# Optimization experiments

Measured on AMD Instinct MI355X. Metric: run time of the kernel, lower is better.

## Reference

```python
import jax, jax.numpy as jnp
import numpy as np

N_EMBD = 1024
NUM_EXPERTS = 8
TOP_K = 2
HIDDEN = 2048  # n_embd * hidden_mult(2)
AUX_COEF = 0.01
B, S = 4, 2048


def setup_inputs() -> dict:
    key = jax.random.key(0)
    k_x, k_g, k_w1, k_w2 = jax.random.split(key, 4)
    x = jax.random.normal(k_x, (B, S, N_EMBD), dtype=jnp.float32)
    # router gate: Linear(n_embd, num_experts, bias=False) -> weight (E, D), applied as x @ W^T
    gate_w = jax.random.uniform(k_g, (NUM_EXPERTS, N_EMBD), dtype=jnp.float32,
                                minval=-1.0 / np.sqrt(N_EMBD), maxval=1.0 / np.sqrt(N_EMBD))
    w1 = jax.random.uniform(k_w1, (NUM_EXPERTS, N_EMBD, HIDDEN), dtype=jnp.float32,
                            minval=-1.0 / np.sqrt(N_EMBD), maxval=1.0 / np.sqrt(N_EMBD))
    w2 = jax.random.uniform(k_w2, (NUM_EXPERTS, HIDDEN, N_EMBD), dtype=jnp.float32,
                            minval=-1.0 / np.sqrt(HIDDEN), maxval=1.0 / np.sqrt(HIDDEN))
    return {"x": x, "gate_w": gate_w, "w1": w1, "w2": w2}


def reference(x, gate_w, w1, w2):
    batch, seq, d = x.shape
    # router (token-level, no noise / eval path)
    router_logits = jnp.einsum('bsd,ed->bse', x, gate_w)          # (B,S,E)
    router_probs = jax.nn.softmax(router_logits, axis=-1)
    top_k_probs, top_k_indices = jax.lax.top_k(router_probs, TOP_K)  # (B,S,K)
    top_k_probs = top_k_probs / jnp.sum(top_k_probs, axis=-1, keepdims=True)

    # dense all-expert FFN (matches torch einsum pattern)
    x_flat = x.reshape(-1, d)                                      # (N,D), N=B*S
    hidden = jnp.einsum('nd,edh->neh', x_flat, w1)                 # (N,E,H)
    hidden = jax.nn.relu(hidden)
    expert_out = jnp.einsum('neh,ehd->ned', hidden, w2)            # (N,E,D)
    expert_out = expert_out.reshape(batch, seq, NUM_EXPERTS, d)    # (B,S,E,D)

    # gather selected experts and combine
    idx = top_k_indices[..., None]                                 # (B,S,K,1)
    selected = jnp.take_along_axis(expert_out, idx, axis=2)        # (B,S,K,D)
    output = jnp.sum(selected * top_k_probs[..., None], axis=2)    # (B,S,D)

    # load-balancing aux loss (Switch style)
    probs_flat = router_probs.reshape(-1, NUM_EXPERTS)             # (N,E)
    top_expert = jnp.argmax(probs_flat, axis=-1)                   # (N,)
    f = jnp.mean(jax.nn.one_hot(top_expert, NUM_EXPERTS, dtype=probs_flat.dtype), axis=0)
    P = jnp.mean(probs_flat, axis=0)
    aux_loss = AUX_COEF * NUM_EXPERTS * jnp.sum(f * P)
    return output, aux_loss
```

## Files before the change

kernel.cpp:

```cpp
#include <hip/hip_runtime.h>
#include <hip/hip_bf16.h>
#include <stdint.h>

#define N_TOK 8192
#define DIM   1024
#define HID   2048
#define NEXP  8
#define RB    256

typedef __bf16 bf16x8 __attribute__((ext_vector_type(8)));
typedef float  f32x4  __attribute__((ext_vector_type(4)));
typedef unsigned short u16x8 __attribute__((ext_vector_type(8)));
typedef unsigned short u16x4 __attribute__((ext_vector_type(4)));

__device__ __forceinline__ float bits2f(unsigned short u) {
    union { unsigned int i; float f; } c; c.i = ((unsigned int)u) << 16; return c.f;
}
__device__ __forceinline__ unsigned short f2bfbits(float f) {
    __hip_bfloat16 h = __float2bfloat16(f);
    return *(unsigned short*)&h;
}

__device__ __forceinline__ void load_lds16(const void* g, void* l) {
    __builtin_amdgcn_global_load_lds(
        (const __attribute__((address_space(1))) void*)g,
        (__attribute__((address_space(3))) void*)l,
        16, 0, 0);
}

#define VMW(Nv) asm volatile("s_waitcnt vmcnt(" #Nv ")" ::: "memory")
#define BARv()  asm volatile("s_barrier" ::: "memory")
#define LGKM0() do { asm volatile("s_waitcnt lgkmcnt(0)" ::: "memory"); \
                     __builtin_amdgcn_sched_barrier(0); } while (0)

__global__ __launch_bounds__(256) void fused_pre_k(
    const float* __restrict__ x,
    const float* __restrict__ gate,
    const float* __restrict__ w1,
    const float* __restrict__ w2,
    int* __restrict__ epack, float* __restrict__ pw,
    unsigned short* __restrict__ xb,
    int* __restrict__ H0, int* __restrict__ H1, float* __restrict__ Pblk,
    unsigned short* __restrict__ w1t, unsigned short* __restrict__ w2t)
{
    __shared__ __align__(16) union {
        struct { float gw[NEXP][16][64]; int h0[NEXP]; int h1[NEXP]; float p[NEXP]; } r;
        unsigned short tile[64][72];
    } S;
    const int tid = threadIdx.x;
    const int bx  = blockIdx.x;

    if (bx < RB) {
        if (tid < NEXP) { S.r.h0[tid] = 0; S.r.h1[tid] = 0; S.r.p[tid] = 0.f; }
        for (int idx = tid; idx < NEXP * DIM; idx += 256) {
            int e = idx >> 10, rem = idx & 1023, i = rem >> 6, l = rem & 63;
            S.r.gw[e][i][l] = gate[e * DIM + l * 16 + i];
        }
        __syncthreads();
        int w = tid >> 6, lane = tid & 63;
        float prAcc[NEXP];
        #pragma unroll
        for (int e = 0; e < NEXP; ++e) prAcc[e] = 0.f;
        for (int it = 0; it < 8; ++it) {
            int token = bx * 32 + w * 8 + it;
            const float* xr = x + (size_t)token * DIM + lane * 16;
            float xv[16];
            #pragma unroll
            for (int q = 0; q < 4; ++q) {
                float4 v = *(const float4*)(xr + q * 4);
                xv[q * 4 + 0] = v.x; xv[q * 4 + 1] = v.y; xv[q * 4 + 2] = v.z; xv[q * 4 + 3] = v.w;
            }
            {
                u16x8 o0, o1;
                #pragma unroll
                for (int i = 0; i < 8; ++i) { o0[i] = f2bfbits(xv[i]); o1[i] = f2bfbits(xv[8 + i]); }
                unsigned short* dst = xb + (size_t)token * DIM + lane * 16;
                *(u16x8*)dst = o0;
                *(u16x8*)(dst + 8) = o1;
            }
            float lg[NEXP];
            #pragma unroll
            for (int e = 0; e < NEXP; ++e) {
                float s = 0.f;
                #pragma unroll
                for (int i = 0; i < 16; ++i) s += xv[i] * S.r.gw[e][i][lane];
                lg[e] = s;
            }
            #pragma unroll
            for (int off = 32; off > 0; off >>= 1)
                #pragma unroll
                for (int e = 0; e < NEXP; ++e) lg[e] += __shfl_xor(lg[e], off);
            float mx = lg[0]; int am = 0;
            #pragma unroll
            for (int e = 1; e < NEXP; ++e) if (lg[e] > mx) { mx = lg[e]; am = e; }
            float pr[NEXP], se = 0.f;
            #pragma unroll
            for (int e = 0; e < NEXP; ++e) { pr[e] = __expf(lg[e] - mx); se += pr[e]; }
            float inv = 1.f / se;
            #pragma unroll
            for (int e = 0; e < NEXP; ++e) pr[e] *= inv;
            float m2 = -1.f; int a2 = 0;
            #pragma unroll
            for (int e = 0; e < NEXP; ++e) if (e != am && pr[e] > m2) { m2 = pr[e]; a2 = e; }
            float psum = pr[am] + m2;
            if (lane == 0) {
                epack[token] = am | (a2 << 4);
                pw[token * 2] = pr[am] / psum;
                pw[token * 2 + 1] = m2 / psum;
                atomicAdd(&S.r.h0[am], 1);
                atomicAdd(&S.r.h1[a2], 1);
                #pragma unroll
                for (int e = 0; e < NEXP; ++e) prAcc[e] += pr[e];
            }
        }
        if (lane == 0) {
            #pragma unroll
            for (int e = 0; e < NEXP; ++e) atomicAdd(&S.r.p[e], prAcc[e]);
        }
        __syncthreads();
        if (tid < NEXP) {
            H0[bx * NEXP + tid] = S.r.h0[tid];
            H1[bx * NEXP + tid] = S.r.h1[tid];
            Pblk[bx * NEXP + tid] = S.r.p[tid];
        }
        return;
    }

    int bT = bx - RB;
    const float* inp; unsigned short* outp;
    int R, C, r0, c0;
    if (bT < 4096) {
        int e = bT >> 9, rem = bT & 511;
        R = DIM; C = HID;
        inp = w1 + (size_t)e * R * C; outp = w1t + (size_t)e * R * C;
        r0 = (rem >> 5) << 6; c0 = (rem & 31) << 6;
    } else {
        int b2 = bT - 4096;
        int e = b2 >> 9, rem = b2 & 511;
        R = HID; C = DIM;
        inp = w2 + (size_t)e * R * C; outp = w2t + (size_t)e * R * C;
        r0 = (rem >> 4) << 6; c0 = (rem & 15) << 6;
    }
    {
        int r = tid >> 2, cseg = (tid & 3) * 16;
        const float* src = inp + (size_t)(r0 + r) * C + c0 + cseg;
        #pragma unroll
        for (int q = 0; q < 4; ++q) {
            float4 v = *(const float4*)(src + q * 4);
            S.tile[r][cseg + q * 4 + 0] = f2bfbits(v.x);
            S.tile[r][cseg + q * 4 + 1] = f2bfbits(v.y);
            S.tile[r][cseg + q * 4 + 2] = f2bfbits(v.z);
            S.tile[r][cseg + q * 4 + 3] = f2bfbits(v.w);
        }
    }
    __syncthreads();
    {
        int c = tid >> 2, rseg = (tid & 3) * 16;
        unsigned short* dst = outp + (size_t)(c0 + c) * R + r0 + rseg;
        #pragma unroll
        for (int h = 0; h < 2; ++h) {
            u16x8 o;
            #pragma unroll
            for (int i = 0; i < 8; ++i) o[i] = S.tile[rseg + h * 8 + i][c];
            *(u16x8*)(dst + h * 8) = o;
        }
    }
}

__global__ __launch_bounds__(256) void scan_k(
    const int* __restrict__ H0, const int* __restrict__ H1,
    const float* __restrict__ Pblk,
    int* __restrict__ bbL, int* __restrict__ counts, int* __restrict__ basep,
    float* __restrict__ aux)
{
    __shared__ int h0S[RB * NEXP], h1S[RB * NEXP], bbS[RB * NEXP];
    __shared__ float pSh[RB * NEXP];
    __shared__ int cS[NEXP], fS[NEXP];
    __shared__ float psS[NEXP];
    int tid = threadIdx.x;
    for (int i = tid; i < RB * NEXP; i += 256) { h0S[i] = H0[i]; h1S[i] = H1[i]; pSh[i] = Pblk[i]; }
    __syncthreads();
    if (tid < NEXP) {
        int run = 0, f = 0; float p = 0.f;
        for (int b = 0; b < RB; ++b) {
            int i = b * NEXP + tid;
            bbS[i] = run;
            run += h0S[i] + h1S[i];
            f += h0S[i];
            p += pSh[i];
        }
        cS[tid] = run; fS[tid] = f; psS[tid] = p;
        counts[tid] = run;
    }
    __syncthreads();
    if (tid == 0) {
        int b = 0; float s = 0.f;
        for (int e = 0; e < NEXP; ++e) {
            basep[e] = b; b += cS[e];
            s += (fS[e] * (1.f / 8192.f)) * (psS[e] * (1.f / 8192.f));
        }
        aux[0] = 0.01f * 8.f * s;
    }
    __syncthreads();
    for (int i = tid; i < RB * NEXP; i += 256) bbL[i] = bbS[i];
}

__global__ __launch_bounds__(256) void scatter_k(
    const int* __restrict__ epack, const int* __restrict__ bbL,
    int* __restrict__ tok_list, int* __restrict__ code)
{
    int tid = threadIdx.x;
    int w = tid >> 6, lane = tid & 63;
    int g = blockIdx.x * 4 + w;
    int token = g * 32 + (lane >> 1);
    int ep = epack[token];
    int e = (lane & 1) ? ((ep >> 4) & 0xF) : (ep & 0xF);
    unsigned long long lower = (lane == 0) ? 0ull : ((~0ull) >> (64 - lane));
    unsigned long long mymask = 0;
    #pragma unroll
    for (int ee = 0; ee < NEXP; ++ee) {
        unsigned long long m = __ballot(e == ee);
        if (ee == e) mymask = m;
    }
    int rank = __popcll(mymask & lower);
    int slot = bbL[g * NEXP + e] + rank;
    tok_list[e * N_TOK + slot] = token;
    code[token * 2 + (lane & 1)] = (e << 13) | slot;
}

template<bool GATHER, bool RELU, int KT, int NTL>
__global__ __launch_bounds__(512, 2) void moe_gemm256(
    const unsigned short* __restrict__ A,
    const unsigned short* __restrict__ B,
    unsigned short* __restrict__ O,
    const int* __restrict__ counts,
    const int* __restrict__ basep,
    const int* __restrict__ tok_list,
    const int N)
{
    constexpr int K = KT * 64;
    const int bid = blockIdx.x;
    const int e  = bid & 7;
    const int q  = bid >> 3;
    const int m0 = (q >> NTL) * 256;
    const int n0 = (q & ((1 << NTL) - 1)) * 256;
    const int cnt = counts[e];
    if (m0 >= cnt) return;
    const int bas = basep[e];

    const int tid = threadIdx.x;
    const int wid = tid >> 6, lane = tid & 63;
    const int wr = wid >> 2, wc = wid & 3;
    const int q4 = lane >> 4, ml = lane & 15;

    __shared__ __align__(16) unsigned short lds[65536];

    const int u  = tid >> 3;
    const int gk = (tid & 7) ^ (u & 7);
    const unsigned short* aR[4];
    #pragma unroll
    for (int g = 0; g < 4; ++g) {
        int slot = m0 + g * 64 + u;
        int row;
        if (GATHER) row = (slot < cnt) ? tok_list[e * N_TOK + slot] : 0;
        else        row = bas + ((slot < cnt) ? slot : (cnt - 1));
        aR[g] = A + (size_t)row * K + gk * 8;
    }
    const unsigned short* Be = B + (size_t)e * (size_t)N * K;
    const unsigned short* bR = Be + (size_t)(n0 + u) * K + gk * 8;
    const int std_ = tid * 8;

    auto stage = [&](int b, int t) {
        const int bo = b * 32768;
        const int tk = t * 64;
        #pragma unroll
        for (int g = 0; g < 4; ++g)
            load_lds16(aR[g] + tk, &lds[bo + g * 4096 + std_]);
        #pragma unroll
        for (int g = 0; g < 4; ++g)
            load_lds16(bR + (size_t)g * 64 * K + tk, &lds[bo + 16384 + g * 4096 + std_]);
    };

    f32x4 acc[8][4];
    #pragma unroll
    for (int i = 0; i < 8; ++i)
        #pragma unroll
        for (int j = 0; j < 4; ++j) acc[i][j] = f32x4{0.f, 0.f, 0.f, 0.f};

    const int cswz = ml & 7;
    const int cp0 = (q4 ^ cswz) * 8;
    const int cp1 = ((4 + q4) ^ cswz) * 8;
    int offA[8], offB[4];
    #pragma unroll
    for (int ii = 0; ii < 8; ++ii) offA[ii] = (wr * 128 + ii * 16 + ml) * 64;
    #pragma unroll
    for (int jj = 0; jj < 4; ++jj) offB[jj] = 16384 + (wc * 64 + jj * 16 + ml) * 64;

    auto compute = [&](int b) {
        const int bo = b * 32768;
        #pragma unroll
        for (int kh = 0; kh < 2; ++kh) {
            const int cp = kh ? cp1 : cp0;
            bf16x8 bF[4];
            #pragma unroll
            for (int jj = 0; jj < 4; ++jj) bF[jj] = *(const bf16x8*)&lds[bo + offB[jj] + cp];
            #pragma unroll
            for (int ii = 0; ii < 8; ++ii) {
                bf16x8 aF = *(const bf16x8*)&lds[bo + offA[ii] + cp];
                __builtin_amdgcn_s_setprio(1);
                #pragma unroll
                for (int jj = 0; jj < 4; ++jj)
                    acc[ii][jj] = __builtin_amdgcn_mfma_f32_16x16x32_bf16(
                        aF, bF[jj], acc[ii][jj], 0, 0, 0);
                __builtin_amdgcn_s_setprio(0);
            }
        }
    };

    stage(0, 0);
    for (int t = 0; t < KT; ++t) {
        const int b = t & 1;
        if (t + 1 < KT) { stage(b ^ 1, t + 1); VMW(8); }
        else            { VMW(0); }
        BARv();
        compute(b);
        LGKM0();
        BARv();
    }

    #pragma unroll
    for (int ii = 0; ii < 8; ++ii) {
        int rbase = wr * 128 + ii * 16 + q4 * 4;
        #pragma unroll
        for (int r = 0; r < 4; ++r) {
            int slot = m0 + rbase + r;
            if (slot < cnt) {
                unsigned short* orow = O + (size_t)(bas + slot) * N + n0 + wc * 64 + ml;
                #pragma unroll
                for (int jj = 0; jj < 4; ++jj) {
                    float v = acc[ii][jj][r];
                    if (RELU) v = v > 0.f ? v : 0.f;
                    orow[jj * 16] = f2bfbits(v);
                }
            }
        }
    }
}

__global__ __launch_bounds__(256) void combine_k(
    const unsigned short* __restrict__ Y,
    const int* __restrict__ code, const float* __restrict__ pw,
    const int* __restrict__ basep,
    float* __restrict__ out)
{
    int t = blockIdx.x;
    int c0 = code[t * 2], c1 = code[t * 2 + 1];
    float p0 = pw[t * 2], p1 = pw[t * 2 + 1];
    size_t r0 = (size_t)(basep[c0 >> 13] + (c0 & 0x1FFF)) * DIM;
    size_t r1 = (size_t)(basep[c1 >> 13] + (c1 & 0x1FFF)) * DIM;
    int d = threadIdx.x * 4;
    u16x4 a = *(const u16x4*)(Y + r0 + d);
    u16x4 b = *(const u16x4*)(Y + r1 + d);
    float4 o;
    o.x = p0 * bits2f(a[0]) + p1 * bits2f(b[0]);
    o.y = p0 * bits2f(a[1]) + p1 * bits2f(b[1]);
    o.z = p0 * bits2f(a[2]) + p1 * bits2f(b[2]);
    o.w = p0 * bits2f(a[3]) + p1 * bits2f(b[3]);
    *(float4*)(out + (size_t)t * DIM + d) = o;
}

extern "C" void kernel_launch(void* const* d_in, const int* in_sizes, int n_in,
                              void* d_out, int out_size, void* d_ws, size_t ws_size,
                              hipStream_t stream)
{
    const float* x    = (const float*)d_in[0];
    const float* gate = (const float*)d_in[1];
    const float* w1   = (const float*)d_in[2];
    const float* w2   = (const float*)d_in[3];
    float* out = (float*)d_out;

    char* ws = (char*)d_ws;
    int*   counts   = (int*)(ws + 0);
    int*   basep    = (int*)(ws + 256);
    int*   epack    = (int*)(ws + 1024);
    int*   H0       = (int*)(ws + 1024 + 32768);
    int*   H1       = (int*)(ws + 1024 + 40960);
    float* Pblk     = (float*)(ws + 1024 + 49152);
    int*   bbL      = (int*)(ws + 1024 + 57344);
    int*   tok_list = (int*)(ws + 131072);
    int*   code     = (int*)(ws + 131072 + 262144);
    float* pw       = (float*)(ws + 131072 + 262144 + 65536);
    unsigned short* w1t    = (unsigned short*)(ws + (1 << 20));
    unsigned short* w2t    = (unsigned short*)(ws + (1 << 20) + 33554432);
    unsigned short* hidden = (unsigned short*)(ws + (1 << 20) + 67108864);
    unsigned short* xb     = (unsigned short*)(ws + (1 << 20) + 134217728);
    unsigned short* Y      = xb;

    fused_pre_k<<<RB + 8192, 256, 0, stream>>>(x, gate, w1, w2, epack, pw, xb,
                                               H0, H1, Pblk, w1t, w2t);
    scan_k<<<1, 256, 0, stream>>>(H0, H1, Pblk, bbL, counts, basep, out + (size_t)N_TOK * DIM);
    scatter_k<<<64, 256, 0, stream>>>(epack, bbL, tok_list, code);
    moe_gemm256<true, true, DIM / 64, 3><<<NEXP * 32 * 8, 512, 0, stream>>>(
        xb, w1t, hidden, counts, basep, tok_list, HID);
    moe_gemm256<false, false, HID / 64, 2><<<NEXP * 32 * 4, 512, 0, stream>>>(
        hidden, w2t, Y, counts, basep, tok_list, DIM);
    combine_k<<<N_TOK, 256, 0, stream>>>(Y, code, pw, basep, out);
}
```

Measured before the change: 425.0 us.

## Split grouped GEMM K-step into quadrant phases interleaving loads and MFMA

```diff
diff --git a/kernel.cpp b/kernel.cpp
--- a/kernel.cpp
+++ b/kernel.cpp
@@ -270,15 +270,21 @@
     const unsigned short* bR = Be + (size_t)(n0 + u) * K + gk * 8;
     const int std_ = tid * 8;
 
-    auto stage = [&](int b, int t) {
-        const int bo = b * 32768;
-        const int tk = t * 64;
-        #pragma unroll
-        for (int g = 0; g < 4; ++g)
-            load_lds16(aR[g] + tk, &lds[bo + g * 4096 + std_]);
-        #pragma unroll
-        for (int g = 0; g < 4; ++g)
-            load_lds16(bR + (size_t)g * 64 * K + tk, &lds[bo + 16384 + g * 4096 + std_]);
+    auto gA01 = [&](int bo_, int t_) {
+        load_lds16(aR[0] + t_ * 64, &lds[bo_ + std_]);
+        load_lds16(aR[1] + t_ * 64, &lds[bo_ + 4096 + std_]);
+    };
+    auto gB01 = [&](int bo_, int t_) {
+        load_lds16(bR + t_ * 64,                    &lds[bo_ + 16384 + std_]);
+        load_lds16(bR + (size_t)64 * K + t_ * 64,   &lds[bo_ + 20480 + std_]);
+    };
+    auto gB23 = [&](int bo_, int t_) {
+        load_lds16(bR + (size_t)128 * K + t_ * 64,  &lds[bo_ + 24576 + std_]);
+        load_lds16(bR + (size_t)192 * K + t_ * 64,  &lds[bo_ + 28672 + std_]);
+    };
+    auto gA23 = [&](int bo_, int t_) {
+        load_lds16(aR[2] + t_ * 64, &lds[bo_ + 8192 + std_]);
+        load_lds16(aR[3] + t_ * 64, &lds[bo_ + 12288 + std_]);
     };
 
     f32x4 acc[8][4];
@@ -290,61 +296,91 @@
     const int cswz = ml & 7;
     const int cp0 = (q4 ^ cswz) * 8;
     const int cp1 = ((4 + q4) ^ cswz) * 8;
-    int offA[8], offB[4];
+    const int aoff = (wr * 64 + ml) * 64;
+    const int boff = 16384 + (wc * 32 + ml) * 64;
+
+    bf16x8 aF[4][2], bF[4][2];
+    auto readA = [&](int bo_, int mh) {
+        #pragma unroll
+        for (int ii = 0; ii < 4; ++ii) {
+            int o = bo_ + aoff + mh * 8192 + ii * 1024;
+            aF[ii][0] = *(const bf16x8*)&lds[o + cp0];
+            aF[ii][1] = *(const bf16x8*)&lds[o + cp1];
+        }
+    };
+    auto readB = [&](int bo_, int nh) {
+        #pragma unroll
+        for (int jj = 0; jj < 2; ++jj) {
+            int o = bo_ + boff + nh * 8192 + jj * 1024;
+            bF[nh * 2 + jj][0] = *(const bf16x8*)&lds[o + cp0];
+            bF[nh * 2 + jj][1] = *(const bf16x8*)&lds[o + cp1];
+        }
+    };
+    auto mm = [&](int mh, int nh) {
+        __builtin_amdgcn_s_setprio(1);
+        #pragma unroll
+        for (int ii = 0; ii < 4; ++ii)
+            #pragma unroll
+            for (int jj = 0; jj < 2; ++jj) {
+                acc[mh * 4 + ii][nh * 2 + jj] = __builtin_amdgcn_mfma_f32_16x16x32_bf16(
+                    aF[ii][0], bF[nh * 2 + jj][0], acc[mh * 4 + ii][nh * 2 + jj], 0, 0, 0);
+                acc[mh * 4 + ii][nh * 2 + jj] = __builtin_amdgcn_mfma_f32_16x16x32_bf16(
+                    aF[ii][1], bF[nh * 2 + jj][1], acc[mh * 4 + ii][nh * 2 + jj], 0, 0, 0);
+            }
+        __builtin_amdgcn_s_setprio(0);
+    };
+
+    gA01(0, 0); gB01(0, 0); gB23(0, 0); gA23(0, 0);
+
+    for (int t = 0; t < KT - 1; ++t) {
+        const int bo = (t & 1) << 15;
+        const int nx = bo ^ 32768;
+        gA01(nx, t + 1); gB01(nx, t + 1);
+        VMW(8); BARv();
+        readA(bo, 0); readB(bo, 0);
+        LGKM0();
+        mm(0, 0);
+        gB23(nx, t + 1);
+        VMW(8); BARv();
+        readB(bo, 1);
+        LGKM0();
+        mm(0, 1);
+        gA23(nx, t + 1);
+        VMW(8); BARv();
+        readA(bo, 1);
+        LGKM0();
+        mm(1, 0);
+        mm(1, 1);
+    }
+    {
+        const int bo = ((KT - 1) & 1) << 15;
+        VMW(4); BARv(); readA(bo, 0); readB(bo, 0); LGKM0(); mm(0, 0);
+        VMW(2); BARv(); readB(bo, 1);               LGKM0(); mm(0, 1);
+        VMW(0); BARv(); readA(bo, 1);               LGKM0(); mm(1, 0);
+        mm(1, 1);
+    }
+
     #pragma unroll
-    for (int ii = 0; ii < 8; ++ii) offA[ii] = (wr * 128 + ii * 16 + ml) * 64;
-    #pragma unroll
-    for (int jj = 0; jj < 4; ++jj) offB[jj] = 16384 + (wc * 64 + jj * 16 + ml) * 64;
-
-    auto compute = [&](int b) {
-        const int bo = b * 32768;
-        #pragma unroll
-        for (int kh = 0; kh < 2; ++kh) {
-            const int cp = kh ? cp1 : cp0;
-            bf16x8 bF[4];
-            #pragma unroll
-            for (int jj = 0; jj < 4; ++jj) bF[jj] = *(const bf16x8*)&lds[bo + offB[jj] + cp];
-            #pragma unroll
-            for (int ii = 0; ii < 8; ++ii) {
-                bf16x8 aF = *(const bf16x8*)&lds[bo + offA[ii] + cp];
-                __builtin_amdgcn_s_setprio(1);
-                #pragma unroll
-                for (int jj = 0; jj < 4; ++jj)
-                    acc[ii][jj] = __builtin_amdgcn_mfma_f32_16x16x32_bf16(
-                        aF, bF[jj], acc[ii][jj], 0, 0, 0);
-                __builtin_amdgcn_s_setprio(0);
-            }
-        }
-    };
-
-    stage(0, 0);
-    for (int t = 0; t < KT; ++t) {
-        const int b = t & 1;
-        if (t + 1 < KT) { stage(b ^ 1, t + 1); VMW(8); }
-        else            { VMW(0); }
-        BARv();
-        compute(b);
-        LGKM0();
-        BARv();
-    }
-
-    #pragma unroll
-    for (int ii = 0; ii < 8; ++ii) {
-        int rbase = wr * 128 + ii * 16 + q4 * 4;
-        #pragma unroll
-        for (int r = 0; r < 4; ++r) {
-            int slot = m0 + rbase + r;
-            if (slot < cnt) {
-                unsigned short* orow = O + (size_t)(bas + slot) * N + n0 + wc * 64 + ml;
-                #pragma unroll
-                for (int jj = 0; jj < 4; ++jj) {
-                    float v = acc[ii][jj][r];
-                    if (RELU) v = v > 0.f ? v : 0.f;
-                    orow[jj * 16] = f2bfbits(v);
+    for (int mh = 0; mh < 2; ++mh)
+        #pragma unroll
+        for (int ii = 0; ii < 4; ++ii) {
+            int rbase = mh * 128 + wr * 64 + ii * 16 + q4 * 4;
+            #pragma unroll
+            for (int r = 0; r < 4; ++r) {
+                int slot = m0 + rbase + r;
+                if (slot < cnt) {
+                    unsigned short* orow = O + (size_t)(bas + slot) * N + n0 + wc * 32 + ml;
+                    #pragma unroll
+                    for (int nh = 0; nh < 2; ++nh)
+                        #pragma unroll
+                        for (int jj = 0; jj < 2; ++jj) {
+                            float v = acc[mh * 4 + ii][nh * 2 + jj][r];
+                            if (RELU) v = v > 0.f ? v : 0.f;
+                            orow[nh * 128 + jj * 16] = f2bfbits(v);
+                        }
                 }
             }
         }
-    }
 }
 
 __global__ __launch_bounds__(256) void combine_k(
```

Result: faster. 395.5 us (-7.0%).
